# Optimization experiments

Hardware: AMD Instinct MI355X
Metric: run time of the kernel (lower is better)

Reference implementation:

```python
import jax, jax.numpy as jnp
import numpy as np

H = 1024      # hidden_size
NH = 16       # num heads
HD = H // NH  # head dim
B, S = 2, 2048


def setup_inputs() -> dict:
    key = jax.random.key(0)
    ks = jax.random.split(key, 10)
    s = 1.0 / np.sqrt(H)
    return {
        "hidden_states": jax.random.normal(ks[0], (B, S, H), dtype=jnp.float32),
        "attention_mask": jax.random.randint(ks[1], (B, S), 0, 2, dtype=jnp.int32),
        "Wq": jax.random.normal(ks[2], (H, H), dtype=jnp.float32) * s,
        "bq": jnp.zeros((H,), dtype=jnp.float32),
        "Wk": jax.random.normal(ks[3], (H, H), dtype=jnp.float32) * s,
        "bk": jnp.zeros((H,), dtype=jnp.float32),
        "Wv": jax.random.normal(ks[4], (H, H), dtype=jnp.float32) * s,
        "bv": jnp.zeros((H,), dtype=jnp.float32),
        "Wo": jax.random.normal(ks[5], (H, H), dtype=jnp.float32) * s,
        "bo": jnp.zeros((H,), dtype=jnp.float32),
    }


def _heads(x):
    # [B,S,H] -> [B,NH,S,HD]
    b, s, _ = x.shape
    return x.reshape(b, s, NH, HD).transpose(0, 2, 1, 3)


def reference(hidden_states, attention_mask, Wq, bq, Wk, bk, Wv, bv, Wo, bo):
    q = _heads(hidden_states @ Wq + bq)
    k = _heads(hidden_states @ Wk + bk)
    v = _heads(hidden_states @ Wv + bv)
    scores = jnp.einsum("bhqd,bhkd->bhqk", q, k) / jnp.sqrt(jnp.float32(HD))
    mask = attention_mask.astype(scores.dtype)[:, None, None, :]  # [B,1,1,S]
    scores = scores + mask * -10000.0
    probs = jax.nn.softmax(scores, axis=-1)  # dropout is identity in eval
    ctx = jnp.einsum("bhqk,bhkd->bhqd", probs, v)
    ctx = ctx.transpose(0, 2, 1, 3).reshape(hidden_states.shape[0], hidden_states.shape[1], H)
    return ctx @ Wo + bo
```

## Files before the change

kernel.cpp:

```cpp
#include <hip/hip_runtime.h>
#include <stdint.h>
#include <stddef.h>

#define S_LEN 2048
#define BATCH 2
#define HID 1024
#define NHEADS 16
#define HDIM 64

typedef __attribute__((ext_vector_type(8))) short short8;
typedef __attribute__((ext_vector_type(4))) short short4v;
typedef __attribute__((ext_vector_type(4))) float float4v;

#define MFMA32(a, b, c) __builtin_amdgcn_mfma_f32_16x16x32_bf16((a), (b), (c), 0, 0, 0)

#if __has_builtin(__builtin_amdgcn_mfma_f32_16x16x16_bf16)
#define MFMA16(a, b, c) __builtin_amdgcn_mfma_f32_16x16x16_bf16((a), (b), (c), 0, 0, 0)
#elif __has_builtin(__builtin_amdgcn_mfma_f32_16x16x16bf16_1k)
#define MFMA16(a, b, c) __builtin_amdgcn_mfma_f32_16x16x16bf16_1k((a), (b), (c), 0, 0, 0)
#else
static __device__ __forceinline__ float4v mfma16_asm(short4v a, short4v b, float4v c) {
  asm volatile("v_mfma_f32_16x16x16_bf16 %0, %1, %2, %0" : "+v"(c) : "v"(a), "v"(b));
  return c;
}
#define MFMA16(a, b, c) mfma16_asm((a), (b), (c))
#endif

#define SCALE_L2E 0.18033688011f

__device__ __forceinline__ short f2bf(float f) {
  union { float f; uint32_t u; } v; v.f = f;
  uint32_t u = v.u;
  uint32_t r = (u + 0x7fffu + ((u >> 16) & 1u)) >> 16;
  return (short)(uint16_t)r;
}

__device__ __forceinline__ short4v pack_bf16x4(float4v v) {
  union { short4v s; uint32_t u[2]; } U;
  U.u[0] = __builtin_amdgcn_perm(__float_as_uint(v[1]) + 0x8000u,
                                 __float_as_uint(v[0]) + 0x8000u, 0x07060302u);
  U.u[1] = __builtin_amdgcn_perm(__float_as_uint(v[3]) + 0x8000u,
                                 __float_as_uint(v[2]) + 0x8000u, 0x07060302u);
  return U.s;
}

__device__ __forceinline__ void gl_lds16(const void* g, void* l) {
  __builtin_amdgcn_global_load_lds((const __attribute__((address_space(1))) void*)g,
                                   (__attribute__((address_space(3))) void*)l,
                                   16, 0, 0);
}

__global__ __launch_bounds__(256) void prep_cast(const float* __restrict__ x,
                                                 const int* __restrict__ mask,
                                                 short* __restrict__ xbf,
                                                 float* __restrict__ maskb) {
  int gid = blockIdx.x * 256 + threadIdx.x;
  const float4v* src = (const float4v*)x;
  float4v v = src[gid];
  short4v o;
  o[0] = f2bf(v[0]); o[1] = f2bf(v[1]); o[2] = f2bf(v[2]); o[3] = f2bf(v[3]);
  ((short4v*)xbf)[gid] = o;
  if (gid < BATCH * S_LEN) maskb[gid] = -14426.9504f * (float)mask[gid];
}

__global__ __launch_bounds__(256) void prep_transpose(const float* __restrict__ w0,
                                                      const float* __restrict__ w1,
                                                      const float* __restrict__ w2,
                                                      const float* __restrict__ w3,
                                                      short* __restrict__ wt) {
  __shared__ short lds[64 * 66];
  int z = blockIdx.z;
  const float* w = (z == 0) ? w0 : (z == 1) ? w1 : (z == 2) ? w2 : w3;
  short* out = wt + (size_t)z * HID * HID;
  int k0 = blockIdx.x * 64, n0 = blockIdx.y * 64;
  int lane = threadIdx.x & 63, wrp = threadIdx.x >> 6;
#pragma unroll
  for (int i = 0; i < 16; i++) {
    int rr = wrp + i * 4;
    lds[lane * 66 + rr] = f2bf(w[(size_t)(k0 + rr) * HID + n0 + lane]);
  }
  __syncthreads();
#pragma unroll
  for (int i = 0; i < 16; i++) {
    int nn = wrp + i * 4;
    out[(size_t)(n0 + nn) * HID + k0 + lane] = lds[nn * 66 + lane];
  }
}

#define VPS 136
template <int BM, int BN, bool TRANS_EP, bool DBUF>
__global__ __launch_bounds__(256) void gemm_bt(const short* __restrict__ A,
                                               const short* __restrict__ WTbase,
                                               const float* __restrict__ bq,
                                               const float* __restrict__ bk,
                                               const float* __restrict__ bv,
                                               const float* __restrict__ bo,
                                               short* __restrict__ outQ,
                                               short* __restrict__ outK,
                                               short* __restrict__ outVt,
                                               float* __restrict__ outF,
                                               int mode_base) {
  constexpr int RI = BM / 32;
  constexpr int RJ = BN / 32;
  constexpr int TILE = BM * 128 + BN * 128;
  constexpr int LSZ1 = DBUF ? TILE * 2 : TILE;
  constexpr int LSZ = (TRANS_EP && LSZ1 < 128 * VPS * 2) ? 128 * VPS * 2 : LSZ1;
  __shared__ __align__(16) char lds[LSZ];
  const int tid = threadIdx.x;
  const int lane = tid & 63, w = tid >> 6;
  const int wm = w & 1, wn = w >> 1;
  const int quad = lane >> 4, l15 = lane & 15;
  const int mode = mode_base + blockIdx.z;
  const short* Bt = WTbase + (size_t)mode * HID * HID;
  const float* bias = (mode == 0) ? bq : (mode == 1) ? bk : (mode == 2) ? bv : bo;
  const int m0 = blockIdx.x * BM, n0 = blockIdx.y * BN;

  float4v acc[RI][RJ];
#pragma unroll
  for (int i = 0; i < RI; i++)
#pragma unroll
    for (int j = 0; j < RJ; j++) acc[i][j] = (float4v)0.0f;

  auto issue = [&](int k0, char* buf) {
#pragma unroll
    for (int inst = 0; inst < BM / 32; inst++) {
      int p = inst * 256 + tid;
      int r = p >> 3;
      int c = (p & 7) ^ (r & 7);
      gl_lds16(A + (size_t)(m0 + r) * HID + k0 + c * 8, buf + p * 16);
    }
#pragma unroll
    for (int inst = 0; inst < BN / 32; inst++) {
      int p = inst * 256 + tid;
      int r = p >> 3;
      int c = (p & 7) ^ (r & 7);
      gl_lds16(Bt + (size_t)(n0 + r) * HID + k0 + c * 8, buf + BM * 128 + p * 16);
    }
  };

  auto compute = [&](const char* buf) {
#pragma unroll
    for (int kk = 0; kk < 2; kk++) {
      short8 af[RI], bf[RJ];
#pragma unroll
      for (int i = 0; i < RI; i++) {
        int ra = wm * (BM / 2) + i * 16 + l15;
        af[i] = *(const short8*)(buf + ra * 128 + (((kk * 4 + quad) ^ (ra & 7)) * 16));
      }
#pragma unroll
      for (int j = 0; j < RJ; j++) {
        int rb = wn * (BN / 2) + j * 16 + l15;
        bf[j] = *(const short8*)(buf + BM * 128 + rb * 128 + (((kk * 4 + quad) ^ (rb & 7)) * 16));
      }
#pragma unroll
      for (int i = 0; i < RI; i++)
#pragma unroll
        for (int j = 0; j < RJ; j++)
          acc[i][j] = MFMA32(af[i], bf[j], acc[i][j]);
    }
  };

  if (DBUF) {
    constexpr int NLD = BM / 32 + BN / 32;
    issue(0, lds);
#pragma unroll 1
    for (int t = 0; t < HID / 64; t++) {
      if (t < HID / 64 - 1) {
        issue((t + 1) * 64, lds + ((t + 1) & 1) * TILE);
        asm volatile("s_waitcnt vmcnt(%0)" ::"i"(NLD) : "memory");
      } else {
        asm volatile("s_waitcnt vmcnt(0)" ::: "memory");
      }
      __builtin_amdgcn_s_barrier();
      asm volatile("" ::: "memory");
      compute(lds + (t & 1) * TILE);
      asm volatile("" ::: "memory");
      __builtin_amdgcn_s_barrier();
    }
  } else {
    for (int k0 = 0; k0 < HID; k0 += 64) {
      __syncthreads();
      issue(k0, lds);
      __syncthreads();
      compute(lds);
    }
  }

  if (TRANS_EP && mode == 2) {
    short* eb = (short*)lds;
    __syncthreads();
#pragma unroll
    for (int j = 0; j < RJ; j++) {
      int nl = wn * (BN / 2) + j * 16 + l15;
      float bsv = bias[n0 + nl];
#pragma unroll
      for (int i = 0; i < RI; i++)
#pragma unroll
        for (int r = 0; r < 4; r++) {
          int ml = wm * (BM / 2) + i * 16 + quad * 4 + r;
          eb[nl * VPS + ml] = f2bf(acc[i][j][r] + bsv);
        }
    }
    __syncthreads();
    int row = tid >> 1, half = tid & 1;
    int n = n0 + row, h = n >> 6, d = n & 63;
    int b = m0 >> 11, sc = (m0 & 2047) + half * 64;
    short* dst = outVt + ((size_t)(b * NHEADS + h) * HDIM + d) * S_LEN + sc;
    const short* src = eb + row * VPS + half * 64;
#pragma unroll
    for (int c = 0; c < 8; c++)
      *(short8*)(dst + c * 8) = *(const short8*)(src + c * 8);
    return;
  }

#pragma unroll
  for (int i = 0; i < RI; i++) {
#pragma unroll
    for (int j = 0; j < RJ; j++) {
      int n = n0 + wn * (BN / 2) + j * 16 + l15;
      float bsv = bias[n];
#pragma unroll
      for (int r = 0; r < 4; r++) {
        int m = m0 + wm * (BM / 2) + i * 16 + quad * 4 + r;
        float val = acc[i][j][r] + bsv;
        if (mode == 3) {
          outF[(size_t)m * HID + n] = val;
        } else {
          int b = m >> 11, s = m & 2047, h = n >> 6, d = n & 63;
          if (mode == 1) val *= SCALE_L2E;
          short u = f2bf(val);
          if (mode == 0)
            outQ[((size_t)(b * NHEADS + h) * S_LEN + s) * HDIM + d] = u;
          else
            outK[((size_t)(b * NHEADS + h) * S_LEN + s) * HDIM + d] = u;
        }
      }
    }
  }
}

#define AT_DB 32768
#define AT_VOFF 16384
#define ALDS_M 65536

__device__ __forceinline__ float* buf_addr(float* base, int row, int col) {
  return base + row * 64 + ((((col >> 2) ^ (row & 15)) << 2) | (col & 3));
}

__global__ __launch_bounds__(256, 2) void attn(const short* __restrict__ Qb,
                                               const short* __restrict__ Kb,
                                               const short* __restrict__ Vt,
                                               const float* __restrict__ maskb,
                                               short* __restrict__ ctx) {
  __shared__ __align__(16) char lds[73728];
  const int tid = threadIdx.x, lane = tid & 63, w = tid >> 6;
  const int quad = lane >> 4, l15 = lane & 15;
  const int h = blockIdx.y, b = blockIdx.z, bh = b * NHEADS + h;
  const short* Qh = Qb + (size_t)bh * S_LEN * HDIM;
  const short* Kh = Kb + (size_t)bh * S_LEN * HDIM;
  const short* Vh = Vt + (size_t)bh * HDIM * S_LEN;
  const float* mbase = maskb + b * S_LEN;
  const int qb0 = blockIdx.x * 64;
  const int kw = w * 32;

  auto issueKV = [&](int kb, int bufi) {
    char* base = lds + bufi * AT_DB;
#pragma unroll
    for (int inst = 0; inst < 4; inst++) {
      int p = inst * 256 + tid;
      int r = p >> 3, c = (p & 7) ^ (r & 7);
      gl_lds16(Kh + (size_t)(kb + r) * HDIM + c * 8, base + p * 16);
      int rv = p >> 4, cv = (p & 15) ^ (rv & 7);
      gl_lds16(Vh + (size_t)rv * S_LEN + kb + cv * 8, base + AT_VOFF + p * 16);
    }
  };

#pragma unroll
  for (int inst = 0; inst < 2; inst++) {
    int p = inst * 256 + tid;
    gl_lds16(mbase + p * 4, lds + ALDS_M + p * 16);
  }
  issueKV(0, 0);

  short8 qf[4][2];
#pragma unroll
  for (int nt = 0; nt < 4; nt++)
#pragma unroll
    for (int kk = 0; kk < 2; kk++)
      qf[nt][kk] = *(const short8*)(Qh + (size_t)(qb0 + nt * 16 + l15) * HDIM + kk * 32 + quad * 8);

  float4v o[4][4];
#pragma unroll
  for (int nt = 0; nt < 4; nt++)
#pragma unroll
    for (int nd = 0; nd < 4; nd++) o[nt][nd] = (float4v)0.0f;
  float lp[4] = {0.0f, 0.0f, 0.0f, 0.0f};

#pragma unroll 1
  for (int kb = 0; kb < S_LEN; kb += 128) {
    const int cur = (kb >> 7) & 1;
    const char* base = lds + cur * AT_DB;
    if (kb + 128 < S_LEN) {
      issueKV(kb + 128, cur ^ 1);
      asm volatile("s_waitcnt vmcnt(%0)" ::"i"(8) : "memory");
    } else {
      asm volatile("s_waitcnt vmcnt(0)" ::: "memory");
    }
    __builtin_amdgcn_s_barrier();
    asm volatile("" ::: "memory");

#pragma unroll
    for (int mt = 0; mt < 2; mt++) {
      short4v bvf[4];
      {
        int g = (kw >> 2) + mt * 4 + quad;
        int gc = g >> 1, sub = g & 1;
#pragma unroll
        for (int nd = 0; nd < 4; nd++) {
          int rv = nd * 16 + l15;
          bvf[nd] = *(const short4v*)(base + AT_VOFF + rv * 256 + ((gc ^ (rv & 7)) * 16) + sub * 8);
        }
      }
      int rk = kw + mt * 16 + l15;
      short8 ka0 = *(const short8*)(base + rk * 128 + ((quad ^ (rk & 7)) * 16));
      short8 ka1 = *(const short8*)(base + rk * 128 + (((4 + quad) ^ (rk & 7)) * 16));
      float4v mbv = *(const float4v*)(lds + ALDS_M + (kb + kw + mt * 16) * 4 + quad * 16);
#pragma unroll
      for (int nt = 0; nt < 4; nt++) {
        float4v c = mbv;
        c = MFMA32(ka0, qf[nt][0], c);
        c = MFMA32(ka1, qf[nt][1], c);
        float4v ev;
#pragma unroll
        for (int r = 0; r < 4; r++) ev[r] = __builtin_amdgcn_exp2f(c[r]);
        lp[nt] += (ev[0] + ev[1]) + (ev[2] + ev[3]);
        short4v ap = pack_bf16x4(ev);
#pragma unroll
        for (int nd = 0; nd < 4; nd++) o[nt][nd] = MFMA16(ap, bvf[nd], o[nt][nd]);
      }
    }
    asm volatile("" ::: "memory");
    __builtin_amdgcn_s_barrier();
  }

#pragma unroll
  for (int nt = 0; nt < 4; nt++) {
    lp[nt] += __shfl_xor(lp[nt], 16, 64);
    lp[nt] += __shfl_xor(lp[nt], 32, 64);
  }
  __syncthreads();
  float* buf0 = (float*)(lds);
  float* buf1 = (float*)(lds + AT_VOFF);
  float* lrowS = (float*)(lds + ALDS_M);
  if (quad == 0) {
#pragma unroll
    for (int nt = 0; nt < 4; nt++) lrowS[w * 64 + nt * 16 + l15] = lp[nt];
  }
  if (w & 1) {
    float* dst = (w == 1) ? buf0 : buf1;
#pragma unroll
    for (int nt = 0; nt < 4; nt++)
#pragma unroll
      for (int nd = 0; nd < 4; nd++)
#pragma unroll
        for (int r = 0; r < 4; r++)
          *buf_addr(dst, nt * 16 + quad * 4 + r, nd * 16 + l15) = o[nt][nd][r];
  }
  __syncthreads();
  if (!(w & 1)) {
    float* srcb = (w == 0) ? buf0 : buf1;
#pragma unroll
    for (int nt = 0; nt < 4; nt++)
#pragma unroll
      for (int nd = 0; nd < 4; nd++)
#pragma unroll
        for (int r = 0; r < 4; r++) {
          float* p = buf_addr(srcb, nt * 16 + quad * 4 + r, nd * 16 + l15);
          *p = *p + o[nt][nd][r];
        }
  }
  __syncthreads();
  int row = w * 16 + l15;
  float ls = lrowS[row] + lrowS[64 + row] + lrowS[128 + row] + lrowS[192 + row];
  float inv = 1.0f / ls;
  short* dstp = ctx + ((size_t)(b * S_LEN + qb0 + row) * HID + h * HDIM + quad * 16);
#pragma unroll
  for (int half = 0; half < 2; half++) {
    int c0 = quad * 16 + half * 8;
    float4v x0 = *(float4v*)buf_addr(buf0, row, c0);
    float4v x1 = *(float4v*)buf_addr(buf0, row, c0 + 4);
    float4v y0 = *(float4v*)buf_addr(buf1, row, c0);
    float4v y1 = *(float4v*)buf_addr(buf1, row, c0 + 4);
    union { short8 s; short4v h[2]; } R;
    float4v s0, s1;
#pragma unroll
    for (int i = 0; i < 4; i++) { s0[i] = (x0[i] + y0[i]) * inv; s1[i] = (x1[i] + y1[i]) * inv; }
    R.h[0] = pack_bf16x4(s0);
    R.h[1] = pack_bf16x4(s1);
    *(short8*)(dstp + half * 8) = R.s;
  }
}

extern "C" void kernel_launch(void* const* d_in, const int* in_sizes, int n_in,
                              void* d_out, int out_size, void* d_ws, size_t ws_size,
                              hipStream_t stream) {
  const float* hs = (const float*)d_in[0];
  const int* mask = (const int*)d_in[1];
  const float* Wq = (const float*)d_in[2];
  const float* bq = (const float*)d_in[3];
  const float* Wk = (const float*)d_in[4];
  const float* bk = (const float*)d_in[5];
  const float* Wv = (const float*)d_in[6];
  const float* bv = (const float*)d_in[7];
  const float* Wo = (const float*)d_in[8];
  const float* bo = (const float*)d_in[9];
  float* out = (float*)d_out;
  char* ws = (char*)d_ws;

  short* XBF = (short*)(ws);
  short* CTX = (short*)(ws);
  short* WT  = (short*)(ws + (size_t)(8u << 20));
  short* QB  = (short*)(ws + (size_t)(16u << 20));
  short* KB  = (short*)(ws + (size_t)(24u << 20));
  short* VTt = (short*)(ws + (size_t)(32u << 20));
  float* MB  = (float*)(ws + (size_t)(40u << 20));

  prep_cast<<<4096, 256, 0, stream>>>(hs, mask, XBF, MB);
  prep_transpose<<<dim3(16, 16, 4), 256, 0, stream>>>(Wq, Wk, Wv, Wo, WT);
  gemm_bt<128, 128, true, true><<<dim3(32, 8, 3), 256, 0, stream>>>(XBF, WT, bq, bk, bv, bo, QB, KB, VTt, nullptr, 0);
  attn<<<dim3(32, NHEADS, BATCH), 256, 0, stream>>>(QB, KB, VTt, MB, CTX);
  gemm_bt<64, 128, false, true><<<dim3(64, 8, 1), 256, 0, stream>>>(CTX, WT, bq, bk, bv, bo, nullptr, nullptr, nullptr, out, 3);
}
```

Measured before the change: 197.4 us.

## Split attention warps 2x2 over queries and keys, halve KV tile for occupancy

Reorganizes the attention block so the four waves form a 2x2 grid: each wave handles 32 query rows against half of a 64-key tile, rather than all 64 query rows against a quarter of a 128-key tile. The KV tile shrinks to 64 keys, cutting LDS from 72KB to 40KB, and launch bounds rise to 4 blocks per CU. The smaller accumulator arrays lower register pressure, and the final cross-wave reduction only has to combine two partial outputs. In exchange there are twice as many loop iterations and barriers, and each K/V fragment loaded from LDS is reused across fewer query tiles.

```diff
diff --git a/kernel.cpp b/kernel.cpp
--- a/kernel.cpp
+++ b/kernel.cpp
@@ -239,39 +239,38 @@
   }
 }
 
-#define AT_DB 32768
-#define AT_VOFF 16384
-#define ALDS_M 65536
+#define AT_DB 16384
+#define AT_VOFF 8192
+#define ALDS_M 32768
 
 __device__ __forceinline__ float* buf_addr(float* base, int row, int col) {
   return base + row * 64 + ((((col >> 2) ^ (row & 15)) << 2) | (col & 3));
 }
 
-__global__ __launch_bounds__(256, 2) void attn(const short* __restrict__ Qb,
+__global__ __launch_bounds__(256, 4) void attn(const short* __restrict__ Qb,
                                                const short* __restrict__ Kb,
                                                const short* __restrict__ Vt,
                                                const float* __restrict__ maskb,
                                                short* __restrict__ ctx) {
-  __shared__ __align__(16) char lds[73728];
+  __shared__ __align__(16) char lds[40960];
   const int tid = threadIdx.x, lane = tid & 63, w = tid >> 6;
   const int quad = lane >> 4, l15 = lane & 15;
+  const int qhalf = w & 1, khalf = w >> 1;
   const int h = blockIdx.y, b = blockIdx.z, bh = b * NHEADS + h;
   const short* Qh = Qb + (size_t)bh * S_LEN * HDIM;
   const short* Kh = Kb + (size_t)bh * S_LEN * HDIM;
   const short* Vh = Vt + (size_t)bh * HDIM * S_LEN;
   const float* mbase = maskb + b * S_LEN;
   const int qb0 = blockIdx.x * 64;
-  const int kw = w * 32;
 
   auto issueKV = [&](int kb, int bufi) {
     char* base = lds + bufi * AT_DB;
 #pragma unroll
-    for (int inst = 0; inst < 4; inst++) {
+    for (int inst = 0; inst < 2; inst++) {
       int p = inst * 256 + tid;
       int r = p >> 3, c = (p & 7) ^ (r & 7);
       gl_lds16(Kh + (size_t)(kb + r) * HDIM + c * 8, base + p * 16);
-      int rv = p >> 4, cv = (p & 15) ^ (rv & 7);
-      gl_lds16(Vh + (size_t)rv * S_LEN + kb + cv * 8, base + AT_VOFF + p * 16);
+      gl_lds16(Vh + (size_t)r * S_LEN + kb + c * 8, base + AT_VOFF + p * 16);
     }
   };
 
@@ -282,27 +281,27 @@
   }
   issueKV(0, 0);
 
-  short8 qf[4][2];
-#pragma unroll
-  for (int nt = 0; nt < 4; nt++)
+  short8 qf[2][2];
+#pragma unroll
+  for (int qt = 0; qt < 2; qt++)
 #pragma unroll
     for (int kk = 0; kk < 2; kk++)
-      qf[nt][kk] = *(const short8*)(Qh + (size_t)(qb0 + nt * 16 + l15) * HDIM + kk * 32 + quad * 8);
-
-  float4v o[4][4];
-#pragma unroll
-  for (int nt = 0; nt < 4; nt++)
-#pragma unroll
-    for (int nd = 0; nd < 4; nd++) o[nt][nd] = (float4v)0.0f;
-  float lp[4] = {0.0f, 0.0f, 0.0f, 0.0f};
+      qf[qt][kk] = *(const short8*)(Qh + (size_t)(qb0 + qhalf * 32 + qt * 16 + l15) * HDIM + kk * 32 + quad * 8);
+
+  float4v o[2][4];
+#pragma unroll
+  for (int qt = 0; qt < 2; qt++)
+#pragma unroll
+    for (int nd = 0; nd < 4; nd++) o[qt][nd] = (float4v)0.0f;
+  float lp[2] = {0.0f, 0.0f};
 
 #pragma unroll 1
-  for (int kb = 0; kb < S_LEN; kb += 128) {
-    const int cur = (kb >> 7) & 1;
+  for (int kb = 0; kb < S_LEN; kb += 64) {
+    const int cur = (kb >> 6) & 1;
     const char* base = lds + cur * AT_DB;
-    if (kb + 128 < S_LEN) {
-      issueKV(kb + 128, cur ^ 1);
-      asm volatile("s_waitcnt vmcnt(%0)" ::"i"(8) : "memory");
+    if (kb + 64 < S_LEN) {
+      issueKV(kb + 64, cur ^ 1);
+      asm volatile("s_waitcnt vmcnt(%0)" ::"i"(4) : "memory");
     } else {
       asm volatile("s_waitcnt vmcnt(0)" ::: "memory");
     }
@@ -313,30 +312,30 @@
     for (int mt = 0; mt < 2; mt++) {
       short4v bvf[4];
       {
-        int g = (kw >> 2) + mt * 4 + quad;
-        int gc = g >> 1, sub = g & 1;
+        int ch = khalf * 4 + mt * 2 + (quad >> 1);
+        int sub = (quad & 1) * 8;
 #pragma unroll
         for (int nd = 0; nd < 4; nd++) {
           int rv = nd * 16 + l15;
-          bvf[nd] = *(const short4v*)(base + AT_VOFF + rv * 256 + ((gc ^ (rv & 7)) * 16) + sub * 8);
+          bvf[nd] = *(const short4v*)(base + AT_VOFF + rv * 128 + ((ch ^ (rv & 7)) * 16) + sub);
         }
       }
-      int rk = kw + mt * 16 + l15;
+      int rk = khalf * 32 + mt * 16 + l15;
       short8 ka0 = *(const short8*)(base + rk * 128 + ((quad ^ (rk & 7)) * 16));
       short8 ka1 = *(const short8*)(base + rk * 128 + (((4 + quad) ^ (rk & 7)) * 16));
-      float4v mbv = *(const float4v*)(lds + ALDS_M + (kb + kw + mt * 16) * 4 + quad * 16);
-#pragma unroll
-      for (int nt = 0; nt < 4; nt++) {
+      float4v mbv = *(const float4v*)(lds + ALDS_M + (kb + khalf * 32 + mt * 16) * 4 + quad * 16);
+#pragma unroll
+      for (int qt = 0; qt < 2; qt++) {
         float4v c = mbv;
-        c = MFMA32(ka0, qf[nt][0], c);
-        c = MFMA32(ka1, qf[nt][1], c);
+        c = MFMA32(ka0, qf[qt][0], c);
+        c = MFMA32(ka1, qf[qt][1], c);
         float4v ev;
 #pragma unroll
         for (int r = 0; r < 4; r++) ev[r] = __builtin_amdgcn_exp2f(c[r]);
-        lp[nt] += (ev[0] + ev[1]) + (ev[2] + ev[3]);
+        lp[qt] += (ev[0] + ev[1]) + (ev[2] + ev[3]);
         short4v ap = pack_bf16x4(ev);
 #pragma unroll
-        for (int nd = 0; nd < 4; nd++) o[nt][nd] = MFMA16(ap, bvf[nd], o[nt][nd]);
+        for (int nd = 0; nd < 4; nd++) o[qt][nd] = MFMA16(ap, bvf[nd], o[qt][nd]);
       }
     }
     asm volatile("" ::: "memory");
@@ -344,57 +343,53 @@
   }
 
 #pragma unroll
-  for (int nt = 0; nt < 4; nt++) {
-    lp[nt] += __shfl_xor(lp[nt], 16, 64);
-    lp[nt] += __shfl_xor(lp[nt], 32, 64);
+  for (int qt = 0; qt < 2; qt++) {
+    lp[qt] += __shfl_xor(lp[qt], 16, 64);
+    lp[qt] += __shfl_xor(lp[qt], 32, 64);
+  }
+  float* lrowS = (float*)(lds + ALDS_M);
+  float* bufP = (float*)(lds + qhalf * 8192);
+  if (quad == 0) {
+#pragma unroll
+    for (int qt = 0; qt < 2; qt++) lrowS[w * 32 + qt * 16 + l15] = lp[qt];
+  }
+  if (khalf == 1) {
+#pragma unroll
+    for (int qt = 0; qt < 2; qt++)
+#pragma unroll
+      for (int nd = 0; nd < 4; nd++)
+#pragma unroll
+        for (int r = 0; r < 4; r++)
+          *buf_addr(bufP, qt * 16 + quad * 4 + r, nd * 16 + l15) = o[qt][nd][r];
   }
   __syncthreads();
-  float* buf0 = (float*)(lds);
-  float* buf1 = (float*)(lds + AT_VOFF);
-  float* lrowS = (float*)(lds + ALDS_M);
-  if (quad == 0) {
-#pragma unroll
-    for (int nt = 0; nt < 4; nt++) lrowS[w * 64 + nt * 16 + l15] = lp[nt];
-  }
-  if (w & 1) {
-    float* dst = (w == 1) ? buf0 : buf1;
-#pragma unroll
-    for (int nt = 0; nt < 4; nt++)
+  if (khalf == 0) {
+#pragma unroll
+    for (int qt = 0; qt < 2; qt++)
 #pragma unroll
       for (int nd = 0; nd < 4; nd++)
 #pragma unroll
-        for (int r = 0; r < 4; r++)
-          *buf_addr(dst, nt * 16 + quad * 4 + r, nd * 16 + l15) = o[nt][nd][r];
-  }
-  __syncthreads();
-  if (!(w & 1)) {
-    float* srcb = (w == 0) ? buf0 : buf1;
-#pragma unroll
-    for (int nt = 0; nt < 4; nt++)
-#pragma unroll
-      for (int nd = 0; nd < 4; nd++)
-#pragma unroll
         for (int r = 0; r < 4; r++) {
-          float* p = buf_addr(srcb, nt * 16 + quad * 4 + r, nd * 16 + l15);
-          *p = *p + o[nt][nd][r];
+          float* p = buf_addr(bufP, qt * 16 + quad * 4 + r, nd * 16 + l15);
+          *p = *p + o[qt][nd][r];
         }
   }
   __syncthreads();
   int row = w * 16 + l15;
-  float ls = lrowS[row] + lrowS[64 + row] + lrowS[128 + row] + lrowS[192 + row];
+  float ls = lrowS[row] + lrowS[64 + row];
   float inv = 1.0f / ls;
+  float* bufq = (float*)(lds + (row >> 5) * 8192);
+  int brow = row & 31;
   short* dstp = ctx + ((size_t)(b * S_LEN + qb0 + row) * HID + h * HDIM + quad * 16);
 #pragma unroll
   for (int half = 0; half < 2; half++) {
     int c0 = quad * 16 + half * 8;
-    float4v x0 = *(float4v*)buf_addr(buf0, row, c0);
-    float4v x1 = *(float4v*)buf_addr(buf0, row, c0 + 4);
-    float4v y0 = *(float4v*)buf_addr(buf1, row, c0);
-    float4v y1 = *(float4v*)buf_addr(buf1, row, c0 + 4);
+    float4v x0 = *(float4v*)buf_addr(bufq, brow, c0);
+    float4v x1 = *(float4v*)buf_addr(bufq, brow, c0 + 4);
     union { short8 s; short4v h[2]; } R;
     float4v s0, s1;
 #pragma unroll
-    for (int i = 0; i < 4; i++) { s0[i] = (x0[i] + y0[i]) * inv; s1[i] = (x1[i] + y1[i]) * inv; }
+    for (int i = 0; i < 4; i++) { s0[i] = x0[i] * inv; s1[i] = x1[i] * inv; }
     R.h[0] = pack_bf16x4(s0);
     R.h[1] = pack_bf16x4(s1);
     *(short8*)(dstp + half * 8) = R.s;
```

Result: faster. 189.0 us (-4.3%).
